# Optimization experiments

Hardware: AMD Instinct MI355X
Metric: run time of the kernel (lower is better)

The kernel has to match this reference:

```python
import math
import jax, jax.numpy as jnp
import numpy as np

# gpt-oss config constants (layer_idx=1 -> sliding_window disabled)
HID = 2880
N_HEADS = 64
N_KV = 8
D_HEAD = 64
GROUPS = N_HEADS // N_KV  # 8 query heads per kv head
SLIDING_WINDOW = 0        # layer_idx % 2 == 1 -> full causal attention
SM_SCALE = 1.0 / math.sqrt(D_HEAD)
EPS = 1e-5

ROPE_BASE = 150000.0
INIT_CTX = 4096
SCALING = 32.0
NTK_ALPHA = 1.0
NTK_BETA = 32.0


def _rope_cos_sin(num_tokens: int):
    """YaRN-scaled RoPE tables, fp32, positions 0..num_tokens-1 (offset=0, no cache)."""
    d_half = D_HEAD // 2
    freq = ROPE_BASE ** (np.arange(0, D_HEAD, 2, dtype=np.float64) / D_HEAD)
    concentration = 0.1 * math.log(SCALING) + 1.0
    low = d_half * math.log(INIT_CTX / (NTK_BETA * 2 * math.pi)) / math.log(ROPE_BASE)
    high = d_half * math.log(INIT_CTX / (NTK_ALPHA * 2 * math.pi)) / math.log(ROPE_BASE)
    interpolation = 1.0 / (SCALING * freq)
    extrapolation = 1.0 / freq
    ramp = (np.arange(d_half, dtype=np.float64) - low) / (high - low)
    mask = 1.0 - np.clip(ramp, 0.0, 1.0)
    inv_freq = interpolation * (1.0 - mask) + extrapolation * mask
    t = np.arange(num_tokens, dtype=np.float64)
    freqs = np.outer(t, inv_freq)  # [S, d_half]
    cos = (np.cos(freqs) * concentration).astype(np.float32)
    sin = (np.sin(freqs) * concentration).astype(np.float32)
    return jnp.asarray(cos), jnp.asarray(sin)


def _rotate(x, cos, sin):
    # x: [B, S, nh, D]; cos/sin: [S, D/2]
    c = cos[None, :, None, :]
    s = sin[None, :, None, :]
    x1, x2 = jnp.split(x, 2, axis=-1)
    return jnp.concatenate([x1 * c - x2 * s, x2 * c + x1 * s], axis=-1)


def setup_inputs() -> dict:
    key = jax.random.key(0)
    ks = jax.random.split(key, 5)
    B, S = 1, 1536
    x = jax.random.normal(ks[0], (B, S, HID), dtype=jnp.float32)
    sinks = jax.random.normal(ks[1], (N_HEADS,), dtype=jnp.float32) * 0.5
    norm_scale = jnp.ones((HID,), dtype=jnp.float32)
    qkv_dim = D_HEAD * (N_HEADS + 2 * N_KV)  # 5120
    qkv_w = jax.random.normal(ks[2], (qkv_dim, HID), dtype=jnp.float32) * 0.02
    qkv_b = jnp.zeros((qkv_dim,), dtype=jnp.float32)
    out_w = jax.random.normal(ks[3], (HID, N_HEADS * D_HEAD), dtype=jnp.float32) * 0.02
    out_b = jnp.zeros((HID,), dtype=jnp.float32)
    return {"x": x, "sinks": sinks, "norm_scale": norm_scale,
            "qkv_w": qkv_w, "qkv_b": qkv_b, "out_w": out_w, "out_b": out_b}


def reference(x, sinks, norm_scale, qkv_w, qkv_b, out_w, out_b):
    B, S, _ = x.shape
    # RMSNorm (fp32)
    t = x * jax.lax.rsqrt(jnp.mean(x * x, axis=-1, keepdims=True) + EPS) * norm_scale
    # fused QKV projection
    qkv = jnp.einsum('bsd,od->bso', t, qkv_w) + qkv_b
    q, k, v = jnp.split(qkv, [N_HEADS * D_HEAD, (N_HEADS + N_KV) * D_HEAD], axis=-1)
    q = q.reshape(B, S, N_HEADS, D_HEAD)
    k = k.reshape(B, S, N_KV, D_HEAD)
    v = v.reshape(B, S, N_KV, D_HEAD)
    # RoPE (offset = 0, no cache)
    cos, sin = _rope_cos_sin(S)
    q = _rotate(q, cos, sin)
    k = _rotate(k, cos, sin)
    # GQA: head h = g*N_KV + kv
    q = q.reshape(B, S, GROUPS, N_KV, D_HEAD)
    scores = jnp.einsum('bqgkd,bskd->bgkqs', q, k) * SM_SCALE  # [B,G,KV,S,S]
    i = jnp.arange(S)[:, None]
    j = jnp.arange(S)[None, :]
    allowed = j <= i  # causal
    if SLIDING_WINDOW > 0:
        allowed = allowed & (i - j < SLIDING_WINDOW)
    scores = jnp.where(allowed[None, None, None, :, :], scores, -1e30)
    # softmax with learned per-head sink logit in the denominator
    sink = sinks.reshape(GROUPS, N_KV)[None, :, :, None]  # [1,G,KV,1]
    m = jnp.maximum(jnp.max(scores, axis=-1), sink)       # [B,G,KV,S]
    p = jnp.exp(scores - m[..., None])
    denom = jnp.sum(p, axis=-1) + jnp.exp(sink - m)
    attn = p / denom[..., None]
    o = jnp.einsum('bgkqs,bskd->bqgkd', attn, v).reshape(B, S, N_HEADS * D_HEAD)
    y = jnp.einsum('bse,oe->bso', o, out_w) + out_b
    return x + y
```

## Files before the change

kernel.cpp:

```cpp
#include <hip/hip_runtime.h>
#include <hip/hip_bf16.h>
#include <math.h>

typedef unsigned short u16;
typedef __attribute__((ext_vector_type(8))) short bf16x8;
typedef __attribute__((ext_vector_type(4))) float f32x4;
typedef __attribute__((ext_vector_type(4))) u16 u16x4;

#define S_LEN   1536
#define HID     2880
#define NH      64
#define NKV     8
#define DH      64
#define QKV_N   5120
#define QDIM    4096
#define KVDIM   512
#define SMSCALE 0.125f
#define EPSV    1e-5f

__device__ __forceinline__ float b2f(u16 u) {
    unsigned int v = ((unsigned int)u) << 16;
    float f; __builtin_memcpy(&f, &v, 4); return f;
}
__device__ __forceinline__ u16 f2b(float f) {
    __hip_bfloat16 h = __float2bfloat16(f);
    return *reinterpret_cast<u16*>(&h);
}
__device__ __forceinline__ void gld16(const u16* g, u16* l) {
    __builtin_amdgcn_global_load_lds(
        (const __attribute__((address_space(1))) unsigned int*)g,
        (__attribute__((address_space(3))) unsigned int*)l, 16, 0, 0);
}
#define WAIT_VM4()   __builtin_amdgcn_s_waitcnt(0xF74)
#define WAIT_VM0()   __builtin_amdgcn_s_waitcnt(0xF70)
#define WAIT_LGKM0() __builtin_amdgcn_s_waitcnt(0xC07F)

__global__ __launch_bounds__(256) void conv_bf16_kernel(
    const float* __restrict__ src, u16* __restrict__ dst, int n4)
{
    int i = blockIdx.x * 256 + threadIdx.x;
    if (i >= n4) return;
    float4 v = ((const float4*)src)[i];
    u16x4 o;
    o.x = f2b(v.x); o.y = f2b(v.y); o.z = f2b(v.z); o.w = f2b(v.w);
    ((u16x4*)dst)[i] = o;
}

__global__ __launch_bounds__(256) void rmsnorm_kernel(
    const float* __restrict__ x, const float* __restrict__ ns, u16* __restrict__ t)
{
    const int s = blockIdx.x;
    const int tid = threadIdx.x;
    const float* xr = x + (size_t)s * HID;
    float ss = 0.f;
    for (int i = tid; i < HID; i += 256) { float v = xr[i]; ss += v * v; }
    for (int off = 32; off > 0; off >>= 1) ss += __shfl_down(ss, off);
    __shared__ float red[4];
    if ((tid & 63) == 0) red[tid >> 6] = ss;
    __syncthreads();
    float tot = red[0] + red[1] + red[2] + red[3];
    float scale = rsqrtf(tot / (float)HID + EPSV);
    u16* tr = t + (size_t)s * HID;
    for (int i = tid; i < HID; i += 256)
        tr[i] = f2b(xr[i] * scale * ns[i]);
}

__global__ __launch_bounds__(256) void rope_table_kernel(float* __restrict__ cosT, float* __restrict__ sinT)
{
    int idx = blockIdx.x * 256 + threadIdx.x;
    if (idx >= S_LEN * 32) return;
    int s = idx >> 5, i = idx & 31;
    const double PI2 = 6.283185307179586476925286766559;
    double base = 150000.0;
    double freq = pow(base, (double)(2 * i) / 64.0);
    double conc = 0.1 * log(32.0) + 1.0;
    double low  = 32.0 * log(4096.0 / (32.0 * PI2)) / log(base);
    double high = 32.0 * log(4096.0 / (1.0  * PI2)) / log(base);
    double interp = 1.0 / (32.0 * freq);
    double extrap = 1.0 / freq;
    double ramp = ((double)i - low) / (high - low);
    double msk = 1.0 - fmin(fmax(ramp, 0.0), 1.0);
    double invf = interp * (1.0 - msk) + extrap * msk;
    double ang = (double)s * invf;
    cosT[idx] = (float)(cos(ang) * conc);
    sinT[idx] = (float)(sin(ang) * conc);
}

__global__ __launch_bounds__(256) void gemm_bt_split_kernel(
    const u16* __restrict__ A, const u16* __restrict__ B, u16* __restrict__ Cp,
    int M, int N, int K, int kchunk, int nq, int mh)
{
    __shared__ __align__(16) u16 sA[2][128 * 32];
    __shared__ __align__(16) u16 sB[2][128 * 32];
    const int tid  = threadIdx.x;
    const int wave = tid >> 6, lane = tid & 63;
    const int quad = lane >> 4, l16 = lane & 15;

    const int lin   = blockIdx.x + gridDim.x * blockIdx.y;
    const int c     = lin & 7, slot = lin >> 3;
    const int strip = slot / mh, mm = slot - strip * mh;
    const int ntile = (c & 3) * nq + strip;
    const int mtile = (c >> 2) * mh + mm;
    const int bm = mtile * 128, bn = ntile * 128;

    const int wm = (wave >> 1) * 64, wn = (wave & 1) * 64;
    const int kb = blockIdx.z * kchunk;
    u16* C = Cp + (size_t)blockIdx.z * M * N;

    const int r0   = wave * 32;
    const int lrow = lane >> 2;
    const int lcol = (lane & 3) * 8;

    const u16* gA0 = A + (size_t)(bm + r0 + lrow) * K + lcol + kb;
    const u16* gA1 = gA0 + (size_t)16 * K;
    int br0 = bn + r0 + lrow;      if (br0 > N - 1) br0 = N - 1;
    int br1 = bn + r0 + 16 + lrow; if (br1 > N - 1) br1 = N - 1;
    const u16* gB0 = B + (size_t)br0 * K + lcol + kb;
    const u16* gB1 = B + (size_t)br1 * K + lcol + kb;

    f32x4 acc[4][4];
    #pragma unroll
    for (int mt = 0; mt < 4; mt++)
        #pragma unroll
        for (int nt = 0; nt < 4; nt++)
            acc[mt][nt] = (f32x4){0.f, 0.f, 0.f, 0.f};

    auto stage = [&](int buf, int koff) {
        gld16(gA0 + koff, &sA[buf][r0 * 32]);
        gld16(gA1 + koff, &sA[buf][(r0 + 16) * 32]);
        gld16(gB0 + koff, &sB[buf][r0 * 32]);
        gld16(gB1 + koff, &sB[buf][(r0 + 16) * 32]);
    };
    auto compute = [&](int buf) {
        bf16x8 av[4], bv[4];
        #pragma unroll
        for (int mt = 0; mt < 4; mt++)
            av[mt] = *(const bf16x8*)(&sA[buf][(wm + mt * 16 + l16) * 32 + quad * 8]);
        #pragma unroll
        for (int nt = 0; nt < 4; nt++)
            bv[nt] = *(const bf16x8*)(&sB[buf][(wn + nt * 16 + l16) * 32 + quad * 8]);
        #pragma unroll
        for (int mt = 0; mt < 4; mt++)
            #pragma unroll
            for (int nt = 0; nt < 4; nt++)
                acc[mt][nt] = __builtin_amdgcn_mfma_f32_16x16x32_bf16(av[mt], bv[nt], acc[mt][nt], 0, 0, 0);
    };

    const int niter = kchunk / 32;
    stage(0, 0);
    int cur = 0;
    for (int i = 0; i < niter - 1; ++i) {
        stage(cur ^ 1, (i + 1) * 32);
        WAIT_VM4();
        __builtin_amdgcn_s_barrier();
        compute(cur);
        WAIT_LGKM0();
        __builtin_amdgcn_s_barrier();
        cur ^= 1;
    }
    WAIT_VM0();
    __builtin_amdgcn_s_barrier();
    compute(cur);

    #pragma unroll
    for (int mt = 0; mt < 4; mt++) {
        #pragma unroll
        for (int nt = 0; nt < 4; nt++) {
            int col = bn + wn + nt * 16 + l16;
            if (col < N) {
                int row0 = bm + wm + mt * 16 + quad * 4;
                #pragma unroll
                for (int r = 0; r < 4; r++)
                    C[(size_t)(row0 + r) * N + col] = f2b(acc[mt][nt][r]);
            }
        }
    }
}

__global__ __launch_bounds__(256) void rope_apply_kernel(
    const u16* __restrict__ p0, const u16* __restrict__ p1, const float* __restrict__ bias,
    const float* __restrict__ cosT, const float* __restrict__ sinT,
    u16* __restrict__ q_r, u16* __restrict__ k_r, u16* __restrict__ v_r)
{
    int idx = blockIdx.x * 256 + threadIdx.x;
    if (idx >= S_LEN * 80 * 64) return;
    int s  = idx / 5120;
    int rem = idx - s * 5120;
    int hh = rem >> 6;
    int i  = rem & 63;
    const u16* r0p = p0 + (size_t)s * QKV_N;
    const u16* r1p = p1 + (size_t)s * QKV_N;
    #define QKVV(o) (b2f(r0p[o]) + b2f(r1p[o]) + bias[o])
    if (hh < 64) {
        int off = hh * 64, j = i & 31;
        float x1 = QKVV(off + j), x2 = QKVV(off + 32 + j);
        float c = cosT[s * 32 + j], sn = sinT[s * 32 + j];
        float val = (i < 32) ? (x1 * c - x2 * sn) : (x2 * c + x1 * sn);
        q_r[(size_t)s * QDIM + off + i] = f2b(val * SMSCALE);
    } else if (hh < 72) {
        int kh = hh - 64, off = QDIM + kh * 64, j = i & 31;
        float x1 = QKVV(off + j), x2 = QKVV(off + 32 + j);
        float c = cosT[s * 32 + j], sn = sinT[s * 32 + j];
        float val = (i < 32) ? (x1 * c - x2 * sn) : (x2 * c + x1 * sn);
        k_r[(size_t)s * KVDIM + kh * 64 + i] = f2b(val);
    } else {
        int vh = hh - 72, off = QDIM + KVDIM + vh * 64;
        v_r[(size_t)s * KVDIM + vh * 64 + i] = f2b(QKVV(off + i));
    }
    #undef QKVV
}

__global__ __launch_bounds__(256) void vt_kernel(
    const u16* __restrict__ v_r, u16* __restrict__ vt)
{
    __shared__ u16 tile[64][72];
    const int s0 = blockIdx.x * 64;
    const int kvh = blockIdx.y;
    const int tid = threadIdx.x;
    const int r = tid >> 3;
    const int c = (tid & 7) * 8;

    #pragma unroll
    for (int rr = 0; rr < 64; rr += 32) {
        uint4 vv = *(const uint4*)(v_r + (size_t)(s0 + r + rr) * KVDIM + kvh * 64 + c);
        const u16* p = (const u16*)&vv;
        #pragma unroll
        for (int j = 0; j < 8; j++) tile[c + j][r + rr] = p[j];
    }
    __syncthreads();
    #pragma unroll
    for (int rr = 0; rr < 64; rr += 32) {
        uint4 ov;
        u16* p = (u16*)&ov;
        #pragma unroll
        for (int j = 0; j < 8; j++) p[j] = tile[r + rr][c + j];
        *(uint4*)(vt + (size_t)(kvh * 64 + r + rr) * S_LEN + s0 + c) = ov;
    }
}

__global__ __launch_bounds__(256) void attn_kernel(
    const u16* __restrict__ q_r, const u16* __restrict__ k_r, const u16* __restrict__ vt,
    const float* __restrict__ sinks, u16* __restrict__ o)
{
    __shared__ __align__(16) u16 sK[64 * 72];
    __shared__ __align__(16) u16 sVt[64 * 72];
    __shared__ __align__(16) u16 sP[4 * 16 * 72];

    const int bx = blockIdx.x, h = blockIdx.y;
    const int kvh = h & 7;
    const int tid = threadIdx.x, wave = tid >> 6, lane = tid & 63;
    const int quad = lane >> 4, l16 = lane & 15;
    const int srow = tid >> 3;
    const int scol = (tid & 7) * 8;
    u16* sPw = sP + wave * 16 * 72;
    const float sinkv = sinks[h];

    for (int phase = 0; phase < 2; ++phase) {
        const int qt = phase ? (23 - bx) : bx;
        const int q_i = qt * 64 + wave * 16 + l16;
        const u16* qp = q_r + (size_t)q_i * QDIM + h * 64 + quad * 8;
        bf16x8 aq0 = *(const bf16x8*)(qp);
        bf16x8 aq1 = *(const bf16x8*)(qp + 32);

        float m_i = sinkv, l_i = 1.0f;
        f32x4 acc[4];
        #pragma unroll
        for (int dt = 0; dt < 4; dt++) acc[dt] = (f32x4){0.f, 0.f, 0.f, 0.f};

        const int kend = qt * 64 + 64;
        for (int j0 = 0; j0 < kend; j0 += 64) {
            __syncthreads();
            #pragma unroll
            for (int rr = 0; rr < 64; rr += 32) {
                *(uint4*)(sK + (srow + rr) * 72 + scol) =
                    *(const uint4*)(k_r + (size_t)(j0 + srow + rr) * KVDIM + kvh * 64 + scol);
                *(uint4*)(sVt + (srow + rr) * 72 + scol) =
                    *(const uint4*)(vt + (size_t)(kvh * 64 + srow + rr) * S_LEN + j0 + scol);
            }
            __syncthreads();

            f32x4 sc[4];
            #pragma unroll
            for (int nt = 0; nt < 4; nt++) {
                const u16* kp = sK + (nt * 16 + l16) * 72 + quad * 8;
                bf16x8 bk0 = *(const bf16x8*)(kp);
                bf16x8 bk1 = *(const bf16x8*)(kp + 32);
                f32x4 s0 = (f32x4){0.f, 0.f, 0.f, 0.f};
                s0 = __builtin_amdgcn_mfma_f32_16x16x32_bf16(bk0, aq0, s0, 0, 0, 0);
                s0 = __builtin_amdgcn_mfma_f32_16x16x32_bf16(bk1, aq1, s0, 0, 0, 0);
                sc[nt] = s0;
            }

            if (j0 + 64 == kend) {
                #pragma unroll
                for (int nt = 0; nt < 4; nt++)
                    #pragma unroll
                    for (int r = 0; r < 4; r++)
                        if (j0 + nt * 16 + quad * 4 + r > q_i) sc[nt][r] = -INFINITY;
            }

            float vmax = sc[0][0];
            #pragma unroll
            for (int nt = 0; nt < 4; nt++)
                #pragma unroll
                for (int r = 0; r < 4; r++) vmax = fmaxf(vmax, sc[nt][r]);
            vmax = fmaxf(vmax, __shfl_xor(vmax, 16));
            vmax = fmaxf(vmax, __shfl_xor(vmax, 32));
            float mnew = fmaxf(m_i, vmax);
            float alpha = __expf(m_i - mnew);
            float ps = 0.f;
            u16x4 pk[4];
            #pragma unroll
            for (int nt = 0; nt < 4; nt++) {
                #pragma unroll
                for (int r = 0; r < 4; r++) {
                    float p = __expf(sc[nt][r] - mnew);
                    ps += p;
                    pk[nt][r] = f2b(p);
                }
            }
            ps += __shfl_xor(ps, 16);
            ps += __shfl_xor(ps, 32);
            l_i = l_i * alpha + ps;
            m_i = mnew;
            #pragma unroll
            for (int nt = 0; nt < 4; nt++)
                *(u16x4*)(sPw + l16 * 72 + nt * 16 + quad * 4) = pk[nt];
            #pragma unroll
            for (int dt = 0; dt < 4; dt++)
                #pragma unroll
                for (int r = 0; r < 4; r++) acc[dt][r] *= alpha;
            __threadfence_block();

            bf16x8 ap0 = *(const bf16x8*)(sPw + l16 * 72 + quad * 8);
            bf16x8 ap1 = *(const bf16x8*)(sPw + l16 * 72 + 32 + quad * 8);
            #pragma unroll
            for (int dt = 0; dt < 4; dt++) {
                const u16* vp = sVt + (dt * 16 + l16) * 72 + quad * 8;
                bf16x8 bv0 = *(const bf16x8*)(vp);
                bf16x8 bv1 = *(const bf16x8*)(vp + 32);
                acc[dt] = __builtin_amdgcn_mfma_f32_16x16x32_bf16(bv0, ap0, acc[dt], 0, 0, 0);
                acc[dt] = __builtin_amdgcn_mfma_f32_16x16x32_bf16(bv1, ap1, acc[dt], 0, 0, 0);
            }
        }

        float inv = 1.0f / l_i;
        #pragma unroll
        for (int dt = 0; dt < 4; dt++) {
            u16x4 ov;
            #pragma unroll
            for (int r = 0; r < 4; r++) ov[r] = f2b(acc[dt][r] * inv);
            *(u16x4*)(o + (size_t)q_i * QDIM + h * 64 + dt * 16 + quad * 4) = ov;
        }
    }
}

__global__ __launch_bounds__(256) void final_add_kernel(
    const u16* __restrict__ p0, const u16* __restrict__ p1,
    const float* __restrict__ bias, const float* __restrict__ x, float* __restrict__ out)
{
    int i = blockIdx.x * 256 + threadIdx.x;
    int base = i * 4;
    int col = base % HID;
    float4 xo = *(const float4*)(x + base);
    float4 bi = *(const float4*)(bias + col);
    u16x4 a = ((const u16x4*)p0)[i];
    u16x4 b = ((const u16x4*)p1)[i];
    float4 r;
    r.x = b2f(a.x) + b2f(b.x) + bi.x + xo.x;
    r.y = b2f(a.y) + b2f(b.y) + bi.y + xo.y;
    r.z = b2f(a.z) + b2f(b.z) + bi.z + xo.z;
    r.w = b2f(a.w) + b2f(b.w) + bi.w + xo.w;
    *(float4*)(out + base) = r;
}

extern "C" void kernel_launch(void* const* d_in, const int* in_sizes, int n_in,
                              void* d_out, int out_size, void* d_ws, size_t ws_size,
                              hipStream_t stream)
{
    const float* x          = (const float*)d_in[0];
    const float* sinks      = (const float*)d_in[1];
    const float* norm_scale = (const float*)d_in[2];
    const float* qkv_w      = (const float*)d_in[3];
    const float* qkv_b      = (const float*)d_in[4];
    const float* out_w      = (const float*)d_in[5];
    const float* out_b      = (const float*)d_in[6];
    float* out = (float*)d_out;

    char* ws = (char*)d_ws;
    u16* t        = (u16*)(ws);
    u16* qkv_w_bf = (u16*)(ws + 8847360);
    u16* qkvp0    = (u16*)(ws + 38338560);
    u16* qkvp1    = (u16*)(ws + 54067200);
    float* cosT   = (float*)(ws + 69795840);
    float* sinT   = (float*)(ws + 69992448);
    u16* k_r      = (u16*)(ws);
    u16* vt       = (u16*)(ws + 1572864);
    u16* q_r      = (u16*)(ws + 3145728);
    u16* o        = (u16*)(ws + 15728640);
    u16* v_r      = (u16*)(ws + 28311552);
    u16* outp0    = (u16*)(ws + 28311552);
    u16* outp1    = (u16*)(ws + 37158912);
    u16* out_w_bf = (u16*)(ws + 46006272);

    rmsnorm_kernel<<<S_LEN, 256, 0, stream>>>(x, norm_scale, t);
    conv_bf16_kernel<<<(QKV_N * HID / 4 + 255) / 256, 256, 0, stream>>>(qkv_w, qkv_w_bf, QKV_N * HID / 4);
    rope_table_kernel<<<(S_LEN * 32) / 256, 256, 0, stream>>>(cosT, sinT);
    gemm_bt_split_kernel<<<dim3(QKV_N / 128, S_LEN / 128, 2), 256, 0, stream>>>(
        t, qkv_w_bf, qkvp0, S_LEN, QKV_N, HID, HID / 2, 10, 6);
    rope_apply_kernel<<<(S_LEN * 80 * 64) / 256, 256, 0, stream>>>(
        qkvp0, qkvp1, qkv_b, cosT, sinT, q_r, k_r, v_r);
    vt_kernel<<<dim3(S_LEN / 64, NKV), 256, 0, stream>>>(v_r, vt);
    conv_bf16_kernel<<<(HID * QDIM / 4 + 255) / 256, 256, 0, stream>>>(out_w, out_w_bf, HID * QDIM / 4);
    attn_kernel<<<dim3(12, NH), 256, 0, stream>>>(q_r, k_r, vt, sinks, o);
    gemm_bt_split_kernel<<<dim3(24, S_LEN / 128, 2), 256, 0, stream>>>(
        o, out_w_bf, outp0, S_LEN, HID, QDIM, QDIM / 2, 6, 6);
    final_add_kernel<<<S_LEN * HID / 4 / 256, 256, 0, stream>>>(outp0, outp1, out_b, x, out);
}
```

Measured before the change: 368.0 us.

## Replace GEMM with 256x256-tile, 8-wave kernel and adjusted split-K

```diff
diff --git a/kernel.cpp b/kernel.cpp
--- a/kernel.cpp
+++ b/kernel.cpp
@@ -31,9 +31,9 @@
         (const __attribute__((address_space(1))) unsigned int*)g,
         (__attribute__((address_space(3))) unsigned int*)l, 16, 0, 0);
 }
+#define WAIT_VM6()   __builtin_amdgcn_s_waitcnt(0xF76)
 #define WAIT_VM4()   __builtin_amdgcn_s_waitcnt(0xF74)
 #define WAIT_VM0()   __builtin_amdgcn_s_waitcnt(0xF70)
-#define WAIT_LGKM0() __builtin_amdgcn_s_waitcnt(0xC07F)
 
 __global__ __launch_bounds__(256) void conv_bf16_kernel(
     const float* __restrict__ src, u16* __restrict__ dst, int n4)
@@ -86,92 +86,123 @@
     sinT[idx] = (float)(sin(ang) * conc);
 }
 
-__global__ __launch_bounds__(256) void gemm_bt_split_kernel(
-    const u16* __restrict__ A, const u16* __restrict__ B, u16* __restrict__ Cp,
-    int M, int N, int K, int kchunk, int nq, int mh)
-{
-    __shared__ __align__(16) u16 sA[2][128 * 32];
-    __shared__ __align__(16) u16 sB[2][128 * 32];
+__global__ __launch_bounds__(512, 2) void gemm_bt_8p_kernel(
+    const u16* __restrict__ A, const u16* __restrict__ B,
+    u16* __restrict__ Cp, u16* __restrict__ Cp2,
+    int M, int N, int K, int it0, int it1, int ntm, int ntn)
+{
+    extern __shared__ __align__(16) u16 smem[];
+    u16* sAp = smem;
+    u16* sBp = smem + 32768;
+
     const int tid  = threadIdx.x;
     const int wave = tid >> 6, lane = tid & 63;
     const int quad = lane >> 4, l16 = lane & 15;
-
-    const int lin   = blockIdx.x + gridDim.x * blockIdx.y;
-    const int c     = lin & 7, slot = lin >> 3;
-    const int strip = slot / mh, mm = slot - strip * mh;
-    const int ntile = (c & 3) * nq + strip;
-    const int mtile = (c >> 2) * mh + mm;
-    const int bm = mtile * 128, bn = ntile * 128;
-
-    const int wm = (wave >> 1) * 64, wn = (wave & 1) * 64;
-    const int kb = blockIdx.z * kchunk;
-    u16* C = Cp + (size_t)blockIdx.z * M * N;
-
-    const int r0   = wave * 32;
-    const int lrow = lane >> 2;
-    const int lcol = (lane & 3) * 8;
-
-    const u16* gA0 = A + (size_t)(bm + r0 + lrow) * K + lcol + kb;
-    const u16* gA1 = gA0 + (size_t)16 * K;
-    int br0 = bn + r0 + lrow;      if (br0 > N - 1) br0 = N - 1;
-    int br1 = bn + r0 + 16 + lrow; if (br1 > N - 1) br1 = N - 1;
-    const u16* gB0 = B + (size_t)br0 * K + lcol + kb;
-    const u16* gB1 = B + (size_t)br1 * K + lcol + kb;
-
-    f32x4 acc[4][4];
+    const int wm = wave >> 2, wn = wave & 3;
+
+    const int nwg  = gridDim.x;
+    const int cpx  = nwg >> 3;
+    const int flat = blockIdx.x;
+    const int swz  = (flat & 7) * cpx + (flat >> 3);
+    const int tpz  = ntm * ntn;
+    const int z    = swz / tpz;
+    const int rem  = swz - z * tpz;
+    const int nt   = rem / ntm;
+    const int mt   = rem - nt * ntm;
+    const int bm = mt * 256, bn = nt * 256;
+    const int niter = z ? it1 : it0;
+    const int kb    = z ? (it0 + (z - 1) * it1) * 64 : 0;
+    u16* C = (z < 2) ? (Cp + (size_t)z * M * N) : Cp2;
+
+    const int r2  = tid >> 2;
+    const int ks8 = (tid & 3) * 8;
+    const u16* gA0 = A + (size_t)(bm + r2) * K + kb + ks8;
+    const u16* gA1 = gA0 + (size_t)128 * K;
+    int brA = bn + r2;       if (brA > N - 1) brA = N - 1;
+    int brB = bn + 128 + r2; if (brB > N - 1) brB = N - 1;
+    const u16* gB0 = B + (size_t)brA * K + kb + ks8;
+    const u16* gB1 = B + (size_t)brB * K + kb + ks8;
+    const int sw = wave * 512;
+
+    f32x4 acc[8][4];
     #pragma unroll
-    for (int mt = 0; mt < 4; mt++)
-        #pragma unroll
-        for (int nt = 0; nt < 4; nt++)
-            acc[mt][nt] = (f32x4){0.f, 0.f, 0.f, 0.f};
-
-    auto stage = [&](int buf, int koff) {
-        gld16(gA0 + koff, &sA[buf][r0 * 32]);
-        gld16(gA1 + koff, &sA[buf][(r0 + 16) * 32]);
-        gld16(gB0 + koff, &sB[buf][r0 * 32]);
-        gld16(gB1 + koff, &sB[buf][(r0 + 16) * 32]);
+    for (int i = 0; i < 8; i++)
+        #pragma unroll
+        for (int j = 0; j < 4; j++) acc[i][j] = (f32x4){0.f, 0.f, 0.f, 0.f};
+
+    auto stA = [&](int c, int kh, int t) {
+        u16* d = sAp + (((c << 1) | kh) << 13);
+        const int koff = t * 64 + kh * 32;
+        gld16(gA0 + koff, d + sw);
+        gld16(gA1 + koff, d + 4096 + sw);
     };
-    auto compute = [&](int buf) {
-        bf16x8 av[4], bv[4];
-        #pragma unroll
-        for (int mt = 0; mt < 4; mt++)
-            av[mt] = *(const bf16x8*)(&sA[buf][(wm + mt * 16 + l16) * 32 + quad * 8]);
-        #pragma unroll
-        for (int nt = 0; nt < 4; nt++)
-            bv[nt] = *(const bf16x8*)(&sB[buf][(wn + nt * 16 + l16) * 32 + quad * 8]);
-        #pragma unroll
-        for (int mt = 0; mt < 4; mt++)
-            #pragma unroll
-            for (int nt = 0; nt < 4; nt++)
-                acc[mt][nt] = __builtin_amdgcn_mfma_f32_16x16x32_bf16(av[mt], bv[nt], acc[mt][nt], 0, 0, 0);
+    auto stB = [&](int c, int kh, int t) {
+        u16* d = sBp + (((c << 1) | kh) << 13);
+        const int koff = t * 64 + kh * 32;
+        gld16(gB0 + koff, d + sw);
+        gld16(gB1 + koff, d + 4096 + sw);
     };
 
-    const int niter = kchunk / 32;
-    stage(0, 0);
-    int cur = 0;
-    for (int i = 0; i < niter - 1; ++i) {
-        stage(cur ^ 1, (i + 1) * 32);
+    bf16x8 bv[4];
+    const int arow = wm * 128 + l16;
+    const int brow = wn * 64 + l16;
+    auto rdB = [&](int c, int ks) {
+        const u16* p = sBp + (((c << 1) | ks) << 13) + brow * 32 + quad * 8;
+        #pragma unroll
+        for (int nf = 0; nf < 4; nf++) bv[nf] = *(const bf16x8*)(p + nf * 16 * 32);
+    };
+    auto mmph = [&](int c, int ks, int mh) {
+        const u16* p = sAp + (((c << 1) | ks) << 13) + (arow + mh * 64) * 32 + quad * 8;
+        bf16x8 av[4];
+        #pragma unroll
+        for (int mf = 0; mf < 4; mf++) av[mf] = *(const bf16x8*)(p + mf * 16 * 32);
+        __builtin_amdgcn_s_setprio(1);
+        #pragma unroll
+        for (int mf = 0; mf < 4; mf++)
+            #pragma unroll
+            for (int nf = 0; nf < 4; nf++)
+                acc[mh * 4 + mf][nf] = __builtin_amdgcn_mfma_f32_16x16x32_bf16(
+                    av[mf], bv[nf], acc[mh * 4 + mf][nf], 0, 0, 0);
+        __builtin_amdgcn_s_setprio(0);
+    };
+
+    stA(0, 0, 0); stB(0, 0, 0); stA(0, 1, 0); stB(0, 1, 0);
+
+    for (int t = 0; t < niter - 1; ++t) {
+        const int c = t & 1;
+        stA(c ^ 1, 0, t + 1);
+        WAIT_VM6();
+        __builtin_amdgcn_s_barrier();
+        rdB(c, 0); mmph(c, 0, 0);
+        stB(c ^ 1, 0, t + 1);
+        mmph(c, 0, 1);
+        stA(c ^ 1, 1, t + 1);
+        WAIT_VM6();
+        __builtin_amdgcn_s_barrier();
+        rdB(c, 1); mmph(c, 1, 0);
+        stB(c ^ 1, 1, t + 1);
+        mmph(c, 1, 1);
+    }
+    {
+        const int c = (niter - 1) & 1;
         WAIT_VM4();
         __builtin_amdgcn_s_barrier();
-        compute(cur);
-        WAIT_LGKM0();
+        rdB(c, 0); mmph(c, 0, 0); mmph(c, 0, 1);
+        WAIT_VM0();
         __builtin_amdgcn_s_barrier();
-        cur ^= 1;
-    }
-    WAIT_VM0();
-    __builtin_amdgcn_s_barrier();
-    compute(cur);
+        rdB(c, 1); mmph(c, 1, 0); mmph(c, 1, 1);
+    }
 
     #pragma unroll
-    for (int mt = 0; mt < 4; mt++) {
-        #pragma unroll
-        for (int nt = 0; nt < 4; nt++) {
-            int col = bn + wn + nt * 16 + l16;
+    for (int im = 0; im < 8; im++) {
+        const int row0 = bm + wm * 128 + im * 16 + quad * 4;
+        #pragma unroll
+        for (int nf = 0; nf < 4; nf++) {
+            const int col = bn + wn * 64 + nf * 16 + l16;
             if (col < N) {
-                int row0 = bm + wm + mt * 16 + quad * 4;
                 #pragma unroll
                 for (int r = 0; r < 4; r++)
-                    C[(size_t)(row0 + r) * N + col] = f2b(acc[mt][nt][r]);
+                    C[(size_t)(row0 + r) * N + col] = f2b(acc[im][nf][r]);
             }
         }
     }
@@ -356,7 +387,7 @@
 }
 
 __global__ __launch_bounds__(256) void final_add_kernel(
-    const u16* __restrict__ p0, const u16* __restrict__ p1,
+    const u16* __restrict__ p0, const u16* __restrict__ p1, const u16* __restrict__ p2,
     const float* __restrict__ bias, const float* __restrict__ x, float* __restrict__ out)
 {
     int i = blockIdx.x * 256 + threadIdx.x;
@@ -366,11 +397,12 @@
     float4 bi = *(const float4*)(bias + col);
     u16x4 a = ((const u16x4*)p0)[i];
     u16x4 b = ((const u16x4*)p1)[i];
+    u16x4 c = ((const u16x4*)p2)[i];
     float4 r;
-    r.x = b2f(a.x) + b2f(b.x) + bi.x + xo.x;
-    r.y = b2f(a.y) + b2f(b.y) + bi.y + xo.y;
-    r.z = b2f(a.z) + b2f(b.z) + bi.z + xo.z;
-    r.w = b2f(a.w) + b2f(b.w) + bi.w + xo.w;
+    r.x = b2f(a.x) + b2f(b.x) + b2f(c.x) + bi.x + xo.x;
+    r.y = b2f(a.y) + b2f(b.y) + b2f(c.y) + bi.y + xo.y;
+    r.z = b2f(a.z) + b2f(b.z) + b2f(c.z) + bi.z + xo.z;
+    r.w = b2f(a.w) + b2f(b.w) + b2f(c.w) + bi.w + xo.w;
     *(float4*)(out + base) = r;
 }
 
@@ -401,19 +433,27 @@
     u16* v_r      = (u16*)(ws + 28311552);
     u16* outp0    = (u16*)(ws + 28311552);
     u16* outp1    = (u16*)(ws + 37158912);
+    u16* outp2    = (u16*)(ws + 3145728);
     u16* out_w_bf = (u16*)(ws + 46006272);
+
+    static bool lds_attr_set = false;
+    if (!lds_attr_set) {
+        hipFuncSetAttribute(reinterpret_cast<const void*>(gemm_bt_8p_kernel),
+                            hipFuncAttributeMaxDynamicSharedMemorySize, 131072);
+        lds_attr_set = true;
+    }
 
     rmsnorm_kernel<<<S_LEN, 256, 0, stream>>>(x, norm_scale, t);
     conv_bf16_kernel<<<(QKV_N * HID / 4 + 255) / 256, 256, 0, stream>>>(qkv_w, qkv_w_bf, QKV_N * HID / 4);
     rope_table_kernel<<<(S_LEN * 32) / 256, 256, 0, stream>>>(cosT, sinT);
-    gemm_bt_split_kernel<<<dim3(QKV_N / 128, S_LEN / 128, 2), 256, 0, stream>>>(
-        t, qkv_w_bf, qkvp0, S_LEN, QKV_N, HID, HID / 2, 10, 6);
+    gemm_bt_8p_kernel<<<240, 512, 131072, stream>>>(
+        t, qkv_w_bf, qkvp0, qkvp0, S_LEN, QKV_N, HID, 23, 22, 6, 20);
     rope_apply_kernel<<<(S_LEN * 80 * 64) / 256, 256, 0, stream>>>(
         qkvp0, qkvp1, qkv_b, cosT, sinT, q_r, k_r, v_r);
     vt_kernel<<<dim3(S_LEN / 64, NKV), 256, 0, stream>>>(v_r, vt);
     conv_bf16_kernel<<<(HID * QDIM / 4 + 255) / 256, 256, 0, stream>>>(out_w, out_w_bf, HID * QDIM / 4);
     attn_kernel<<<dim3(12, NH), 256, 0, stream>>>(q_r, k_r, vt, sinks, o);
-    gemm_bt_split_kernel<<<dim3(24, S_LEN / 128, 2), 256, 0, stream>>>(
-        o, out_w_bf, outp0, S_LEN, HID, QDIM, QDIM / 2, 6, 6);
-    final_add_kernel<<<S_LEN * HID / 4 / 256, 256, 0, stream>>>(outp0, outp1, out_b, x, out);
-}
+    gemm_bt_8p_kernel<<<216, 512, 131072, stream>>>(
+        o, out_w_bf, outp0, outp2, S_LEN, HID, QDIM, 22, 21, 6, 12);
+    final_add_kernel<<<S_LEN * HID / 4 / 256, 256, 0, stream>>>(outp0, outp1, outp2, out_b, x, out);
+}
```

Result: faster. 335.4 us (-8.8%).
